# Kernel tuning notes

Hardware: AMD Instinct MI355X
Metric: run time of the kernel (lower is better)

The kernel has to match this reference:

```python
import jax, jax.numpy as jnp
import numpy as np

B, W, H, C = 8, 32, 32, 64   # batch, width, height, hidden_size
NH = 8                        # num_attention_heads
M = 32                        # max_position_embeddings
P = C // 2                    # position_embedding_size (query_positional_score=True)


def setup_inputs() -> dict:
    key = jax.random.key(0)
    ks = jax.random.split(key, 7)
    s = 0.02
    return {
        "hidden_states": jax.random.normal(ks[0], (B, W, H, C), dtype=jnp.float32),
        "row_emb": jax.random.normal(ks[1], (2 * M - 1, P), dtype=jnp.float32) * s,
        "col_emb": jax.random.normal(ks[2], (2 * M - 1, P), dtype=jnp.float32) * s,
        "Wq": jax.random.normal(ks[3], (NH * C, C), dtype=jnp.float32) * s,
        "bq": jnp.zeros((NH * C,), dtype=jnp.float32),
        "Wk": jax.random.normal(ks[4], (NH * C, C), dtype=jnp.float32) * s,
        "bk": jnp.zeros((NH * C,), dtype=jnp.float32),
        "Wv": jax.random.normal(ks[5], (C, NH * C), dtype=jnp.float32) * s,
        "bv": jnp.zeros((C,), dtype=jnp.float32),
    }


def reference(hidden_states, row_emb, col_emb, Wq, bq, Wk, bk, Wv, bv):
    b, w, h, c = hidden_states.shape
    nh = Wq.shape[0] // c
    half = c // 2
    center = row_emb.shape[0] // 2  # = max_position_embeddings - 1

    # projections: all_head_size = nh * c (per source: hidden_size * num_heads)
    q = (hidden_states @ Wq.T + bq).reshape(b, w, h, nh, c)
    k = (hidden_states @ Wk.T + bk).reshape(b, w, h, nh, c)

    # relative index tables: rel[i, j] = (j - i) + (M - 1)
    iw = jnp.arange(w)
    ih = jnp.arange(h)
    rel_w = iw[None, :] - iw[:, None] + center   # (w, w)
    rel_h = ih[None, :] - ih[:, None] + center   # (h, h)
    r_emb = row_emb[rel_w]  # (w, w, P)
    c_emb = col_emb[rel_h]  # (h, h, P)

    # positional scores: q split into row/col halves
    q_row = q[..., :half]
    q_col = q[..., half:]
    row_scores = jnp.einsum('bijhd,ikd->bijhk', q_row, r_emb)  # (b,w,h,nh,w)
    col_scores = jnp.einsum('bijhd,jld->bijhl', q_col, c_emb)  # (b,w,h,nh,h)
    scale = jnp.sqrt(jnp.asarray(c, dtype=hidden_states.dtype))
    scores = (row_scores[..., :, None] + col_scores[..., None, :]) / scale  # (b,w,h,nh,w,h)

    # content scores q^T k
    scores = scores + jnp.einsum('bijhd,bklhd->bijhkl', q, k) / scale

    # softmax over merged spatial key dims (k,l)
    probs = jax.nn.softmax(scores.reshape(b, w, h, nh, w * h), axis=-1).reshape(scores.shape)

    # value mixing directly with hidden_states, then output projection
    mixed = jnp.einsum('bijhkl,bkld->bijhd', probs, hidden_states).reshape(b, w, h, nh * c)
    return mixed @ Wv.T + bv
```

## Files before the change

### kernel.cpp

```cpp
#include <hip/hip_runtime.h>
#include <math.h>

typedef __bf16 bf16;
typedef bf16 bf16x2 __attribute__((ext_vector_type(2)));
typedef bf16 bf16x4 __attribute__((ext_vector_type(4)));
typedef bf16 bf16x8 __attribute__((ext_vector_type(8)));
typedef float f32x4 __attribute__((ext_vector_type(4)));

constexpr int CENTER = 31;

static __device__ __forceinline__ unsigned short f2bf_bits(float f) {
    bf16 b = (bf16)f;
    return __builtin_bit_cast(unsigned short, b);
}

__global__ __launch_bounds__(256)
void prep_kernel(const float* __restrict__ hid,
                 const float* __restrict__ Wq, const float* __restrict__ Wk,
                 const float* __restrict__ Wv,
                 bf16* __restrict__ hb, bf16* __restrict__ htb,
                 bf16* __restrict__ Wqb, bf16* __restrict__ Wkb,
                 bf16* __restrict__ Wvb)
{
    __shared__ __attribute__((aligned(16))) bf16 hs[64][72];

    const int t   = threadIdx.x;
    const int blk = blockIdx.x;
    const int b   = blk >> 4, kc = blk & 15;

    {
        int row = t >> 2, c4 = (t & 3) * 16;
        const float4* src = (const float4*)(hid + ((size_t)b * 1024 + kc * 64 + row) * 64 + c4);
        bf16 tmp[16];
        #pragma unroll
        for (int u = 0; u < 4; ++u) {
            float4 v = src[u];
            tmp[4*u+0] = (bf16)v.x; tmp[4*u+1] = (bf16)v.y;
            tmp[4*u+2] = (bf16)v.z; tmp[4*u+3] = (bf16)v.w;
        }
        *(int4*)&hs[row][c4]     = ((int4*)tmp)[0];
        *(int4*)&hs[row][c4 + 8] = ((int4*)tmp)[1];
        bf16* hdst = hb + ((size_t)b * 1024 + kc * 64 + row) * 64 + c4;
        *(int4*)hdst       = ((int4*)tmp)[0];
        *(int4*)(hdst + 8) = ((int4*)tmp)[1];
    }

    {
        int idx = blk * 256 + t;
        if (idx < 8192) {
            float4 vq = ((const float4*)Wq)[idx];
            float4 vk = ((const float4*)Wk)[idx];
            float4 vv = ((const float4*)Wv)[idx];
            ushort4 pq, pk2, pv;
            pq.x = f2bf_bits(vq.x); pq.y = f2bf_bits(vq.y); pq.z = f2bf_bits(vq.z); pq.w = f2bf_bits(vq.w);
            pk2.x = f2bf_bits(vk.x); pk2.y = f2bf_bits(vk.y); pk2.z = f2bf_bits(vk.z); pk2.w = f2bf_bits(vk.w);
            pv.x = f2bf_bits(vv.x); pv.y = f2bf_bits(vv.y); pv.z = f2bf_bits(vv.z); pv.w = f2bf_bits(vv.w);
            ((ushort4*)Wqb)[idx] = pq;
            ((ushort4*)Wkb)[idx] = pk2;
            ((ushort4*)Wvb)[idx] = pv;
        }
    }
    __syncthreads();

    {
        int d = t >> 2, p0 = (t & 3) * 16;
        ushort tmp[16];
        #pragma unroll
        for (int i = 0; i < 16; ++i)
            tmp[i] = __builtin_bit_cast(unsigned short, hs[p0 + i][d]);
        bf16* dst = htb + ((size_t)b * 64 + d) * 1024 + kc * 64 + p0;
        *(int4*)dst       = ((int4*)tmp)[0];
        *(int4*)(dst + 8) = ((int4*)tmp)[1];
    }
}

__global__ __launch_bounds__(256)
void qkproj_kernel(const bf16* __restrict__ hb,
                   const bf16* __restrict__ Wqb, const float* __restrict__ bq,
                   const bf16* __restrict__ Wkb, const float* __restrict__ bk,
                   bf16* __restrict__ qb, bf16* __restrict__ kb)
{
    __shared__ __attribute__((aligned(16))) bf16 As[128][72];
    __shared__ __attribute__((aligned(16))) bf16 Bqs[128][72];
    __shared__ __attribute__((aligned(16))) bf16 Bks[128][72];

    const int t  = threadIdx.x;
    const int pt = blockIdx.x;
    const int ot = blockIdx.y;
    const int p0 = pt * 128;
    const int b  = p0 >> 10;

    {
        int row = t >> 1, ch = (t & 1) * 32;
        const int4* asrc = (const int4*)(hb + (size_t)(p0 + row) * 64 + ch);
        const int4* qsrc = (const int4*)(Wqb + (size_t)(ot * 128 + row) * 64 + ch);
        const int4* ksrc = (const int4*)(Wkb + (size_t)(ot * 128 + row) * 64 + ch);
        #pragma unroll
        for (int u = 0; u < 4; ++u) {
            *(int4*)&As[row][ch + u * 8]  = asrc[u];
            *(int4*)&Bqs[row][ch + u * 8] = qsrc[u];
            *(int4*)&Bks[row][ch + u * 8] = ksrc[u];
        }
    }
    __syncthreads();

    const int w = t >> 6, ln = t & 63, l15 = ln & 15, quad = ln >> 4;

    bf16x8 a[2][2];
    #pragma unroll
    for (int mt = 0; mt < 2; ++mt) {
        a[mt][0] = *(const bf16x8*)&As[w * 32 + mt * 16 + l15][quad * 8];
        a[mt][1] = *(const bf16x8*)&As[w * 32 + mt * 16 + l15][32 + quad * 8];
    }

    const f32x4 z4 = {0.f, 0.f, 0.f, 0.f};

    for (int z = 0; z < 2; ++z) {
        const bf16 (* __restrict__ Bs)[72] = z ? Bks : Bqs;
        const float* bias = z ? bk : bq;
        bf16* outp        = z ? kb : qb;
        const float scale = z ? 1.0f : 0.125f;

        f32x4 acc[2][8];
        #pragma unroll
        for (int mt = 0; mt < 2; ++mt)
            #pragma unroll
            for (int nt = 0; nt < 8; ++nt) acc[mt][nt] = z4;

        #pragma unroll
        for (int nt = 0; nt < 8; ++nt) {
            bf16x8 b0 = *(const bf16x8*)&Bs[nt * 16 + l15][quad * 8];
            bf16x8 b1 = *(const bf16x8*)&Bs[nt * 16 + l15][32 + quad * 8];
            #pragma unroll
            for (int mt = 0; mt < 2; ++mt) {
                acc[mt][nt] = __builtin_amdgcn_mfma_f32_16x16x32_bf16(a[mt][0], b0, acc[mt][nt], 0, 0, 0);
                acc[mt][nt] = __builtin_amdgcn_mfma_f32_16x16x32_bf16(a[mt][1], b1, acc[mt][nt], 0, 0, 0);
            }
        }

        #pragma unroll
        for (int nt = 0; nt < 8; ++nt) {
            int o = ot * 128 + nt * 16 + l15;
            float bv = bias[o];
            int hh = o >> 6, d = o & 63;
            #pragma unroll
            for (int mt = 0; mt < 2; ++mt)
                #pragma unroll
                for (int r = 0; r < 4; ++r) {
                    int pos = (p0 & 1023) + w * 32 + mt * 16 + quad * 4 + r;
                    float val = (acc[mt][nt][r] + bv) * scale;
                    outp[(((size_t)b * 8 + hh) * 1024 + pos) * 64 + d] = (bf16)val;
                }
        }
    }
}

__global__ __launch_bounds__(256)
void bias_kernel(const bf16* __restrict__ qb,
                 const float* __restrict__ row_emb, const float* __restrict__ col_emb,
                 bf16* __restrict__ rowbias, bf16* __restrict__ colbias)
{
    __shared__ __attribute__((aligned(16))) bf16 embRs[63][40];
    __shared__ __attribute__((aligned(16))) bf16 embCs[63][40];

    const int t  = threadIdx.x;
    const int bh = blockIdx.x;
    const int sg = blockIdx.y;

    for (int i = t; i < 2016; i += 256) embRs[i >> 5][i & 31] = (bf16)row_emb[i];
    for (int i = t; i < 2016; i += 256) embCs[i >> 5][i & 31] = (bf16)col_emb[i];
    __syncthreads();

    const int w = t >> 6, ln = t & 63, l15 = ln & 15, quad = ln >> 4;

    #pragma unroll
    for (int u = 0; u < 4; ++u) {
        int s = sg * 16 + u * 4 + w;
        bool cm = s >= 32;
        int ij = cm ? s - 32 : s;

        bf16x8 a[2];
        #pragma unroll
        for (int mt = 0; mt < 2; ++mt) {
            const bf16* ap = cm
                ? qb + ((size_t)bh * 1024 + (mt * 16 + l15) * 32 + ij) * 64 + 32 + quad * 8
                : qb + ((size_t)bh * 1024 + ij * 32 + mt * 16 + l15) * 64 + quad * 8;
            a[mt] = *(const bf16x8*)ap;
        }
        bf16* ob = cm ? colbias : rowbias;

        #pragma unroll
        for (int nt = 0; nt < 2; ++nt) {
            int erow = nt * 16 + l15 + CENTER - ij;
            bf16x8 bfrag = cm ? *(const bf16x8*)&embCs[erow][quad * 8]
                              : *(const bf16x8*)&embRs[erow][quad * 8];
            #pragma unroll
            for (int mt = 0; mt < 2; ++mt) {
                f32x4 c = {0.f, 0.f, 0.f, 0.f};
                c = __builtin_amdgcn_mfma_f32_16x16x32_bf16(a[mt], bfrag, c, 0, 0, 0);
                #pragma unroll
                for (int r = 0; r < 4; ++r) {
                    int ql = mt * 16 + quad * 4 + r;
                    int qrow = cm ? ql * 32 + ij : ij * 32 + ql;
                    ob[((size_t)bh * 1024 + qrow) * 32 + nt * 16 + l15] = (bf16)c[r];
                }
            }
        }
    }
}

__global__ __launch_bounds__(256, 2)
void attn_kernel(const bf16* __restrict__ qb, const bf16* __restrict__ kb,
                 const bf16* __restrict__ htb,
                 const bf16* __restrict__ rowbias, const bf16* __restrict__ colbias,
                 bf16* __restrict__ mixedb)
{
    __shared__ __attribute__((aligned(16))) bf16 Ks[64][72];
    __shared__ __attribute__((aligned(16))) bf16 Hts[64][72];
    __shared__ __attribute__((aligned(16))) bf16 Pp[4][32][72];

    const int t  = threadIdx.x;
    const int qt = blockIdx.x;
    const int bh = blockIdx.y;
    const int b  = bh >> 3, h = bh & 7;
    const int q0 = qt * 128;
    const int w = t >> 6, ln = t & 63, l15 = ln & 15, quad = ln >> 4;

    bf16x8 bq_[2][2];
    float  cbv[2][2][4];
    const bf16* rbp[2];
    #pragma unroll
    for (int mt = 0; mt < 2; ++mt) {
        int qrow = q0 + w * 32 + mt * 16 + l15;
        const bf16* qp = qb + ((size_t)bh * 1024 + qrow) * 64;
        bq_[mt][0] = *(const bf16x8*)(qp + quad * 8);
        bq_[mt][1] = *(const bf16x8*)(qp + 32 + quad * 8);
        #pragma unroll
        for (int par = 0; par < 2; ++par) {
            bf16x4 cv = *(const bf16x4*)(colbias + ((size_t)bh * 1024 + qrow) * 32 + par * 16 + quad * 4);
            #pragma unroll
            for (int r = 0; r < 4; ++r) cbv[mt][par][r] = (float)cv[r];
        }
        rbp[mt] = rowbias + ((size_t)bh * 1024 + qrow) * 32;
    }

    const f32x4 z4 = {0.f, 0.f, 0.f, 0.f};
    f32x4 oacc[2][4];
    float lsum[2] = {0.f, 0.f};
    #pragma unroll
    for (int mt = 0; mt < 2; ++mt)
        #pragma unroll
        for (int dt = 0; dt < 4; ++dt) oacc[mt][dt] = z4;

    bf16* Pw = &Pp[w][0][0];
    const bf16* kcbase = kb + (size_t)bh * 1024 * 64;
    const bf16* hcbase = htb + (size_t)b * 64 * 1024;

    for (int kc = 0; kc < 16; ++kc) {
        __syncthreads();
        {
            int row = t >> 2, c = (t & 3) << 4;
            const bf16* ksrc = kcbase + (size_t)(kc * 64 + row) * 64 + c;
            *(int4*)&Ks[row][c]     = *(const int4*)ksrc;
            *(int4*)&Ks[row][c + 8] = *(const int4*)(ksrc + 8);
            const bf16* hsrc = hcbase + (size_t)row * 1024 + kc * 64 + c;
            *(int4*)&Hts[row][c]     = *(const int4*)hsrc;
            *(int4*)&Hts[row][c + 8] = *(const int4*)(hsrc + 8);
        }
        float rb[2][2];
        #pragma unroll
        for (int mt = 0; mt < 2; ++mt) {
            bf16x2 rv = *(const bf16x2*)(rbp[mt] + kc * 2);
            rb[mt][0] = (float)rv[0]; rb[mt][1] = (float)rv[1];
        }
        __syncthreads();

        f32x4 sf[2][4];
        #pragma unroll
        for (int mt = 0; mt < 2; ++mt)
            #pragma unroll
            for (int kt = 0; kt < 4; ++kt) sf[mt][kt] = z4;
        #pragma unroll
        for (int kt = 0; kt < 4; ++kt) {
            bf16x8 aK0 = *(const bf16x8*)&Ks[kt * 16 + l15][quad * 8];
            bf16x8 aK1 = *(const bf16x8*)&Ks[kt * 16 + l15][32 + quad * 8];
            #pragma unroll
            for (int mt = 0; mt < 2; ++mt) {
                sf[mt][kt] = __builtin_amdgcn_mfma_f32_16x16x32_bf16(aK0, bq_[mt][0], sf[mt][kt], 0, 0, 0);
                sf[mt][kt] = __builtin_amdgcn_mfma_f32_16x16x32_bf16(aK1, bq_[mt][1], sf[mt][kt], 0, 0, 0);
            }
        }

        #pragma unroll
        for (int mt = 0; mt < 2; ++mt)
            #pragma unroll
            for (int kt = 0; kt < 4; ++kt) {
                float rbv = rb[mt][kt >> 1];
                ushort4 pk;
                float p0 = __expf(sf[mt][kt][0] + rbv + cbv[mt][kt & 1][0]);
                float p1 = __expf(sf[mt][kt][1] + rbv + cbv[mt][kt & 1][1]);
                float p2 = __expf(sf[mt][kt][2] + rbv + cbv[mt][kt & 1][2]);
                float p3 = __expf(sf[mt][kt][3] + rbv + cbv[mt][kt & 1][3]);
                lsum[mt] += (p0 + p1) + (p2 + p3);
                pk.x = f2bf_bits(p0); pk.y = f2bf_bits(p1);
                pk.z = f2bf_bits(p2); pk.w = f2bf_bits(p3);
                *(ushort4*)&Pw[(mt * 16 + l15) * 72 + kt * 16 + quad * 4] = pk;
            }

        bf16x8 bp[2][2];
        #pragma unroll
        for (int mt = 0; mt < 2; ++mt) {
            bp[mt][0] = *(const bf16x8*)&Pw[(mt * 16 + l15) * 72 + quad * 8];
            bp[mt][1] = *(const bf16x8*)&Pw[(mt * 16 + l15) * 72 + 32 + quad * 8];
        }
        #pragma unroll
        for (int dt = 0; dt < 4; ++dt) {
            bf16x8 aH0 = *(const bf16x8*)&Hts[dt * 16 + l15][quad * 8];
            bf16x8 aH1 = *(const bf16x8*)&Hts[dt * 16 + l15][32 + quad * 8];
            #pragma unroll
            for (int mt = 0; mt < 2; ++mt) {
                oacc[mt][dt] = __builtin_amdgcn_mfma_f32_16x16x32_bf16(aH0, bp[mt][0], oacc[mt][dt], 0, 0, 0);
                oacc[mt][dt] = __builtin_amdgcn_mfma_f32_16x16x32_bf16(aH1, bp[mt][1], oacc[mt][dt], 0, 0, 0);
            }
        }
    }

    float inv[2];
    #pragma unroll
    for (int mt = 0; mt < 2; ++mt) {
        float v = lsum[mt];
        v += __shfl_xor(v, 16);
        v += __shfl_xor(v, 32);
        inv[mt] = 1.0f / v;
    }
    #pragma unroll
    for (int mt = 0; mt < 2; ++mt) {
        int pos = q0 + w * 32 + mt * 16 + l15;
        bf16* mb = mixedb + ((size_t)b * 1024 + pos) * 512 + h * 64;
        #pragma unroll
        for (int dt = 0; dt < 4; ++dt) {
            ushort4 pk;
            pk.x = f2bf_bits(oacc[mt][dt][0] * inv[mt]);
            pk.y = f2bf_bits(oacc[mt][dt][1] * inv[mt]);
            pk.z = f2bf_bits(oacc[mt][dt][2] * inv[mt]);
            pk.w = f2bf_bits(oacc[mt][dt][3] * inv[mt]);
            *(ushort4*)(mb + dt * 16 + quad * 4) = pk;
        }
    }
}

__global__ __launch_bounds__(256)
void out_proj_kernel(const bf16* __restrict__ mixedb,
                     const bf16* __restrict__ Wvb, const float* __restrict__ bv,
                     float* __restrict__ out)
{
    __shared__ __attribute__((aligned(16))) bf16 Wvs[64][264];

    const int t  = threadIdx.x;
    const int p0 = blockIdx.x * 64;
    const int w = t >> 6, ln = t & 63, l15 = ln & 15, quad = ln >> 4;

    f32x4 acc[4];
    #pragma unroll
    for (int nt = 0; nt < 4; ++nt) {
        float bvv = bv[nt * 16 + l15];
        acc[nt] = (f32x4){bvv, bvv, bvv, bvv};
    }

    const bf16* arow = mixedb + (size_t)(p0 + w * 16 + l15) * 512;

    for (int half = 0; half < 2; ++half) {
        __syncthreads();
        {
            int c = t >> 2, seg = (t & 3) * 64;
            const int4* src = (const int4*)(Wvb + (size_t)c * 512 + half * 256 + seg);
            #pragma unroll
            for (int u = 0; u < 8; ++u)
                *(int4*)&Wvs[c][seg + u * 8] = src[u];
        }
        __syncthreads();

        #pragma unroll
        for (int kc = 0; kc < 8; ++kc) {
            bf16x8 a = *(const bf16x8*)(arow + half * 256 + kc * 32 + quad * 8);
            #pragma unroll
            for (int nt = 0; nt < 4; ++nt) {
                bf16x8 bfrag = *(const bf16x8*)&Wvs[nt * 16 + l15][kc * 32 + quad * 8];
                acc[nt] = __builtin_amdgcn_mfma_f32_16x16x32_bf16(a, bfrag, acc[nt], 0, 0, 0);
            }
        }
    }

    #pragma unroll
    for (int nt = 0; nt < 4; ++nt)
        #pragma unroll
        for (int r = 0; r < 4; ++r)
            out[(size_t)(p0 + w * 16 + quad * 4 + r) * 64 + nt * 16 + l15] = acc[nt][r];
}

extern "C" void kernel_launch(void* const* d_in, const int* in_sizes, int n_in,
                              void* d_out, int out_size, void* d_ws, size_t ws_size,
                              hipStream_t stream)
{
    const float* hid     = (const float*)d_in[0];
    const float* row_emb = (const float*)d_in[1];
    const float* col_emb = (const float*)d_in[2];
    const float* Wq      = (const float*)d_in[3];
    const float* bq      = (const float*)d_in[4];
    const float* Wk      = (const float*)d_in[5];
    const float* bk      = (const float*)d_in[6];
    const float* Wv      = (const float*)d_in[7];
    const float* bv      = (const float*)d_in[8];
    float* out = (float*)d_out;

    bf16* qb      = (bf16*)d_ws;
    bf16* kb      = qb + (size_t)64 * 1024 * 64;
    bf16* htb     = kb + (size_t)64 * 1024 * 64;
    bf16* rowbias = htb + (size_t)8 * 64 * 1024;
    bf16* colbias = rowbias + (size_t)64 * 1024 * 32;
    bf16* mixedb  = colbias + (size_t)64 * 1024 * 32;
    bf16* hb      = mixedb + (size_t)8 * 1024 * 512;
    bf16* Wqb     = hb + (size_t)8 * 1024 * 64;
    bf16* Wkb     = Wqb + (size_t)512 * 64;
    bf16* Wvb     = Wkb + (size_t)512 * 64;

    prep_kernel<<<128, 256, 0, stream>>>(hid, Wq, Wk, Wv, hb, htb, Wqb, Wkb, Wvb);
    qkproj_kernel<<<dim3(64, 4), 256, 0, stream>>>(hb, Wqb, bq, Wkb, bk, qb, kb);
    bias_kernel<<<dim3(64, 4), 256, 0, stream>>>(qb, row_emb, col_emb, rowbias, colbias);
    attn_kernel<<<dim3(8, 64), 256, 0, stream>>>(qb, kb, htb, rowbias, colbias, mixedb);
    out_proj_kernel<<<128, 256, 0, stream>>>(mixedb, Wvb, bv, out);
}
```

Measured before the change: 131.5 us.

## Pre-pack H and Wv into MFMA fragment layout, double-buffer K tiles in attention

The prep kernel now writes the transposed hidden states and Wv in a fragment-packed layout, so each lane can load its MFMA operands straight from global memory. The attention kernel drops the shared-memory staging of H, double-buffers the K tiles with a register prefetch, needs only one barrier per iteration, and preloads all row-bias values once. out_proj removes its shared-memory Wv staging and uses smaller tiles over twice as many blocks. In exchange, H fragments are read redundantly from global memory (or cache) by every wave, and register pressure rises.

```diff
diff --git a/kernel.cpp b/kernel.cpp
--- a/kernel.cpp
+++ b/kernel.cpp
@@ -18,9 +18,9 @@
 void prep_kernel(const float* __restrict__ hid,
                  const float* __restrict__ Wq, const float* __restrict__ Wk,
                  const float* __restrict__ Wv,
-                 bf16* __restrict__ hb, bf16* __restrict__ htb,
+                 bf16* __restrict__ hb, bf16* __restrict__ htp,
                  bf16* __restrict__ Wqb, bf16* __restrict__ Wkb,
-                 bf16* __restrict__ Wvb)
+                 bf16* __restrict__ Wvp)
 {
     __shared__ __attribute__((aligned(16))) bf16 hs[64][72];
 
@@ -57,18 +57,22 @@
             pv.x = f2bf_bits(vv.x); pv.y = f2bf_bits(vv.y); pv.z = f2bf_bits(vv.z); pv.w = f2bf_bits(vv.w);
             ((ushort4*)Wqb)[idx] = pq;
             ((ushort4*)Wkb)[idx] = pk2;
-            ((ushort4*)Wvb)[idx] = pv;
+            int c = idx >> 7, o4 = (idx & 127) * 4;
+            size_t dst = (size_t)((c >> 4) * 16 + (o4 >> 5)) * 512 + (c & 15) * 32 + (o4 & 31);
+            *(ushort4*)(Wvp + dst) = pv;
         }
     }
     __syncthreads();
 
     {
-        int d = t >> 2, p0 = (t & 3) * 16;
+        int d = t >> 2, seg = (t & 3) * 16;
+        int dt = d >> 4, l15 = d & 15, half = seg >> 5;
         ushort tmp[16];
         #pragma unroll
         for (int i = 0; i < 16; ++i)
-            tmp[i] = __builtin_bit_cast(unsigned short, hs[p0 + i][d]);
-        bf16* dst = htb + ((size_t)b * 64 + d) * 1024 + kc * 64 + p0;
+            tmp[i] = __builtin_bit_cast(unsigned short, hs[seg + i][d]);
+        bf16* dst = htp + (size_t)b * 65536 + kc * 4096 + dt * 1024
+                        + half * 512 + l15 * 32 + (seg & 31);
         *(int4*)dst       = ((int4*)tmp)[0];
         *(int4*)(dst + 8) = ((int4*)tmp)[1];
     }
@@ -211,12 +215,11 @@
 
 __global__ __launch_bounds__(256, 2)
 void attn_kernel(const bf16* __restrict__ qb, const bf16* __restrict__ kb,
-                 const bf16* __restrict__ htb,
+                 const bf16* __restrict__ htp,
                  const bf16* __restrict__ rowbias, const bf16* __restrict__ colbias,
                  bf16* __restrict__ mixedb)
 {
-    __shared__ __attribute__((aligned(16))) bf16 Ks[64][72];
-    __shared__ __attribute__((aligned(16))) bf16 Hts[64][72];
+    __shared__ __attribute__((aligned(16))) bf16 Ks[2][64][72];
     __shared__ __attribute__((aligned(16))) bf16 Pp[4][32][72];
 
     const int t  = threadIdx.x;
@@ -228,7 +231,7 @@
 
     bf16x8 bq_[2][2];
     float  cbv[2][2][4];
-    const bf16* rbp[2];
+    bf16x8 rb8[2][4];
     #pragma unroll
     for (int mt = 0; mt < 2; ++mt) {
         int qrow = q0 + w * 32 + mt * 16 + l15;
@@ -241,7 +244,9 @@
             #pragma unroll
             for (int r = 0; r < 4; ++r) cbv[mt][par][r] = (float)cv[r];
         }
-        rbp[mt] = rowbias + ((size_t)bh * 1024 + qrow) * 32;
+        const bf16* rp = rowbias + ((size_t)bh * 1024 + qrow) * 32;
+        #pragma unroll
+        for (int u = 0; u < 4; ++u) rb8[mt][u] = *(const bf16x8*)(rp + u * 8);
     }
 
     const f32x4 z4 = {0.f, 0.f, 0.f, 0.f};
@@ -253,27 +258,36 @@
         for (int dt = 0; dt < 4; ++dt) oacc[mt][dt] = z4;
 
     bf16* Pw = &Pp[w][0][0];
-    const bf16* kcbase = kb + (size_t)bh * 1024 * 64;
-    const bf16* hcbase = htb + (size_t)b * 64 * 1024;
-
+    const bf16* kcbase = kb + (size_t)bh * 65536;
+    const bf16* hfrag  = htp + (size_t)b * 65536 + l15 * 32 + quad * 8;
+
+    const int srow = t >> 2, sc = (t & 3) << 4;
+    {
+        const bf16* ks0 = kcbase + (size_t)srow * 64 + sc;
+        *(int4*)&Ks[0][srow][sc]     = *(const int4*)ks0;
+        *(int4*)&Ks[0][srow][sc + 8] = *(const int4*)(ks0 + 8);
+    }
+    __syncthreads();
+
+    #pragma unroll 2
     for (int kc = 0; kc < 16; ++kc) {
-        __syncthreads();
+        const int cur = kc & 1, nxt = cur ^ 1;
+
+        int4 kpa, kpb;
+        if (kc < 15) {
+            const bf16* kpre = kcbase + (size_t)((kc + 1) * 64 + srow) * 64 + sc;
+            kpa = *(const int4*)kpre;
+            kpb = *(const int4*)(kpre + 8);
+        }
+        bf16x8 hA[4][2];
         {
-            int row = t >> 2, c = (t & 3) << 4;
-            const bf16* ksrc = kcbase + (size_t)(kc * 64 + row) * 64 + c;
-            *(int4*)&Ks[row][c]     = *(const int4*)ksrc;
-            *(int4*)&Ks[row][c + 8] = *(const int4*)(ksrc + 8);
-            const bf16* hsrc = hcbase + (size_t)row * 1024 + kc * 64 + c;
-            *(int4*)&Hts[row][c]     = *(const int4*)hsrc;
-            *(int4*)&Hts[row][c + 8] = *(const int4*)(hsrc + 8);
-        }
-        float rb[2][2];
-        #pragma unroll
-        for (int mt = 0; mt < 2; ++mt) {
-            bf16x2 rv = *(const bf16x2*)(rbp[mt] + kc * 2);
-            rb[mt][0] = (float)rv[0]; rb[mt][1] = (float)rv[1];
-        }
-        __syncthreads();
+            const bf16* hp = hfrag + kc * 4096;
+            #pragma unroll
+            for (int dt = 0; dt < 4; ++dt) {
+                hA[dt][0] = *(const bf16x8*)(hp + dt * 1024);
+                hA[dt][1] = *(const bf16x8*)(hp + dt * 1024 + 512);
+            }
+        }
 
         f32x4 sf[2][4];
         #pragma unroll
@@ -282,8 +296,8 @@
             for (int kt = 0; kt < 4; ++kt) sf[mt][kt] = z4;
         #pragma unroll
         for (int kt = 0; kt < 4; ++kt) {
-            bf16x8 aK0 = *(const bf16x8*)&Ks[kt * 16 + l15][quad * 8];
-            bf16x8 aK1 = *(const bf16x8*)&Ks[kt * 16 + l15][32 + quad * 8];
+            bf16x8 aK0 = *(const bf16x8*)&Ks[cur][kt * 16 + l15][quad * 8];
+            bf16x8 aK1 = *(const bf16x8*)&Ks[cur][kt * 16 + l15][32 + quad * 8];
             #pragma unroll
             for (int mt = 0; mt < 2; ++mt) {
                 sf[mt][kt] = __builtin_amdgcn_mfma_f32_16x16x32_bf16(aK0, bq_[mt][0], sf[mt][kt], 0, 0, 0);
@@ -292,10 +306,12 @@
         }
 
         #pragma unroll
-        for (int mt = 0; mt < 2; ++mt)
+        for (int mt = 0; mt < 2; ++mt) {
+            float rb0 = (float)rb8[mt][kc >> 2][(kc & 3) * 2];
+            float rb1 = (float)rb8[mt][kc >> 2][(kc & 3) * 2 + 1];
             #pragma unroll
             for (int kt = 0; kt < 4; ++kt) {
-                float rbv = rb[mt][kt >> 1];
+                float rbv = (kt & 2) ? rb1 : rb0;
                 ushort4 pk;
                 float p0 = __expf(sf[mt][kt][0] + rbv + cbv[mt][kt & 1][0]);
                 float p1 = __expf(sf[mt][kt][1] + rbv + cbv[mt][kt & 1][1]);
@@ -306,6 +322,7 @@
                 pk.z = f2bf_bits(p2); pk.w = f2bf_bits(p3);
                 *(ushort4*)&Pw[(mt * 16 + l15) * 72 + kt * 16 + quad * 4] = pk;
             }
+        }
 
         bf16x8 bp[2][2];
         #pragma unroll
@@ -315,14 +332,18 @@
         }
         #pragma unroll
         for (int dt = 0; dt < 4; ++dt) {
-            bf16x8 aH0 = *(const bf16x8*)&Hts[dt * 16 + l15][quad * 8];
-            bf16x8 aH1 = *(const bf16x8*)&Hts[dt * 16 + l15][32 + quad * 8];
             #pragma unroll
             for (int mt = 0; mt < 2; ++mt) {
-                oacc[mt][dt] = __builtin_amdgcn_mfma_f32_16x16x32_bf16(aH0, bp[mt][0], oacc[mt][dt], 0, 0, 0);
-                oacc[mt][dt] = __builtin_amdgcn_mfma_f32_16x16x32_bf16(aH1, bp[mt][1], oacc[mt][dt], 0, 0, 0);
-            }
-        }
+                oacc[mt][dt] = __builtin_amdgcn_mfma_f32_16x16x32_bf16(hA[dt][0], bp[mt][0], oacc[mt][dt], 0, 0, 0);
+                oacc[mt][dt] = __builtin_amdgcn_mfma_f32_16x16x32_bf16(hA[dt][1], bp[mt][1], oacc[mt][dt], 0, 0, 0);
+            }
+        }
+
+        if (kc < 15) {
+            *(int4*)&Ks[nxt][srow][sc]     = kpa;
+            *(int4*)&Ks[nxt][srow][sc + 8] = kpb;
+        }
+        __syncthreads();
     }
 
     float inv[2];
@@ -351,51 +372,34 @@
 
 __global__ __launch_bounds__(256)
 void out_proj_kernel(const bf16* __restrict__ mixedb,
-                     const bf16* __restrict__ Wvb, const float* __restrict__ bv,
+                     const bf16* __restrict__ Wvp, const float* __restrict__ bv,
                      float* __restrict__ out)
 {
-    __shared__ __attribute__((aligned(16))) bf16 Wvs[64][264];
-
     const int t  = threadIdx.x;
-    const int p0 = blockIdx.x * 64;
+    const int p0 = blockIdx.x * 32;
     const int w = t >> 6, ln = t & 63, l15 = ln & 15, quad = ln >> 4;
 
-    f32x4 acc[4];
-    #pragma unroll
-    for (int nt = 0; nt < 4; ++nt) {
-        float bvv = bv[nt * 16 + l15];
-        acc[nt] = (f32x4){bvv, bvv, bvv, bvv};
-    }
-
-    const bf16* arow = mixedb + (size_t)(p0 + w * 16 + l15) * 512;
-
-    for (int half = 0; half < 2; ++half) {
-        __syncthreads();
-        {
-            int c = t >> 2, seg = (t & 3) * 64;
-            const int4* src = (const int4*)(Wvb + (size_t)c * 512 + half * 256 + seg);
-            #pragma unroll
-            for (int u = 0; u < 8; ++u)
-                *(int4*)&Wvs[c][seg + u * 8] = src[u];
-        }
-        __syncthreads();
-
-        #pragma unroll
-        for (int kc = 0; kc < 8; ++kc) {
-            bf16x8 a = *(const bf16x8*)(arow + half * 256 + kc * 32 + quad * 8);
-            #pragma unroll
-            for (int nt = 0; nt < 4; ++nt) {
-                bf16x8 bfrag = *(const bf16x8*)&Wvs[nt * 16 + l15][kc * 32 + quad * 8];
-                acc[nt] = __builtin_amdgcn_mfma_f32_16x16x32_bf16(a, bfrag, acc[nt], 0, 0, 0);
-            }
-        }
-    }
-
-    #pragma unroll
-    for (int nt = 0; nt < 4; ++nt)
+    float bvv = bv[w * 16 + l15];
+    f32x4 acc[2] = {(f32x4){bvv, bvv, bvv, bvv}, (f32x4){bvv, bvv, bvv, bvv}};
+
+    const bf16* arow0 = mixedb + (size_t)(p0 + l15) * 512 + quad * 8;
+    const bf16* arow1 = mixedb + (size_t)(p0 + 16 + l15) * 512 + quad * 8;
+    const bf16* bbase = Wvp + (size_t)w * 16 * 512 + l15 * 32 + quad * 8;
+
+    #pragma unroll
+    for (int kc = 0; kc < 16; ++kc) {
+        bf16x8 a0 = *(const bf16x8*)(arow0 + kc * 32);
+        bf16x8 a1 = *(const bf16x8*)(arow1 + kc * 32);
+        bf16x8 bfrag = *(const bf16x8*)(bbase + kc * 512);
+        acc[0] = __builtin_amdgcn_mfma_f32_16x16x32_bf16(a0, bfrag, acc[0], 0, 0, 0);
+        acc[1] = __builtin_amdgcn_mfma_f32_16x16x32_bf16(a1, bfrag, acc[1], 0, 0, 0);
+    }
+
+    #pragma unroll
+    for (int mt = 0; mt < 2; ++mt)
         #pragma unroll
         for (int r = 0; r < 4; ++r)
-            out[(size_t)(p0 + w * 16 + quad * 4 + r) * 64 + nt * 16 + l15] = acc[nt][r];
+            out[(size_t)(p0 + mt * 16 + quad * 4 + r) * 64 + w * 16 + l15] = acc[mt][r];
 }
 
 extern "C" void kernel_launch(void* const* d_in, const int* in_sizes, int n_in,
@@ -415,18 +419,18 @@
 
     bf16* qb      = (bf16*)d_ws;
     bf16* kb      = qb + (size_t)64 * 1024 * 64;
-    bf16* htb     = kb + (size_t)64 * 1024 * 64;
-    bf16* rowbias = htb + (size_t)8 * 64 * 1024;
+    bf16* htp     = kb + (size_t)64 * 1024 * 64;
+    bf16* rowbias = htp + (size_t)8 * 64 * 1024;
     bf16* colbias = rowbias + (size_t)64 * 1024 * 32;
     bf16* mixedb  = colbias + (size_t)64 * 1024 * 32;
     bf16* hb      = mixedb + (size_t)8 * 1024 * 512;
     bf16* Wqb     = hb + (size_t)8 * 1024 * 64;
     bf16* Wkb     = Wqb + (size_t)512 * 64;
-    bf16* Wvb     = Wkb + (size_t)512 * 64;
-
-    prep_kernel<<<128, 256, 0, stream>>>(hid, Wq, Wk, Wv, hb, htb, Wqb, Wkb, Wvb);
+    bf16* Wvp     = Wkb + (size_t)512 * 64;
+
+    prep_kernel<<<128, 256, 0, stream>>>(hid, Wq, Wk, Wv, hb, htp, Wqb, Wkb, Wvp);
     qkproj_kernel<<<dim3(64, 4), 256, 0, stream>>>(hb, Wqb, bq, Wkb, bk, qb, kb);
     bias_kernel<<<dim3(64, 4), 256, 0, stream>>>(qb, row_emb, col_emb, rowbias, colbias);
-    attn_kernel<<<dim3(8, 64), 256, 0, stream>>>(qb, kb, htb, rowbias, colbias, mixedb);
-    out_proj_kernel<<<128, 256, 0, stream>>>(mixedb, Wvb, bv, out);
-}
+    attn_kernel<<<dim3(8, 64), 256, 0, stream>>>(qb, kb, htp, rowbias, colbias, mixedb);
+    out_proj_kernel<<<256, 256, 0, stream>>>(mixedb, Wvp, bv, out);
+}
```

After: 203.4 us. +54.7%, slower.

## Pre-pack Wv into MFMA fragment layout and drop LDS staging in output projection

Applied to the files above, without the earlier changes.

The prep kernel now writes bf16 Wv in a packed layout of 16-row by 32-column tiles, so each MFMA B fragment becomes one contiguous 16-byte global load. The output projection kernel drops the shared-memory staging of Wv and its barriers, reads fragments directly from global memory and L2, and gives each wave a 16-column output slice over 32 rows. The grid doubles to 256 blocks of 32 rows each to raise parallelism. In exchange, each mixedb row is now read by all four waves rather than once.

```diff
diff --git a/kernel.cpp b/kernel.cpp
--- a/kernel.cpp
+++ b/kernel.cpp
@@ -20,7 +20,7 @@
                  const float* __restrict__ Wv,
                  bf16* __restrict__ hb, bf16* __restrict__ htb,
                  bf16* __restrict__ Wqb, bf16* __restrict__ Wkb,
-                 bf16* __restrict__ Wvb)
+                 bf16* __restrict__ Wvp)
 {
     __shared__ __attribute__((aligned(16))) bf16 hs[64][72];
 
@@ -57,7 +57,9 @@
             pv.x = f2bf_bits(vv.x); pv.y = f2bf_bits(vv.y); pv.z = f2bf_bits(vv.z); pv.w = f2bf_bits(vv.w);
             ((ushort4*)Wqb)[idx] = pq;
             ((ushort4*)Wkb)[idx] = pk2;
-            ((ushort4*)Wvb)[idx] = pv;
+            int c = idx >> 7, o4 = (idx & 127) * 4;
+            size_t dst = (size_t)((c >> 4) * 16 + (o4 >> 5)) * 512 + (c & 15) * 32 + (o4 & 31);
+            *(ushort4*)(Wvp + dst) = pv;
         }
     }
     __syncthreads();
@@ -351,51 +353,34 @@
 
 __global__ __launch_bounds__(256)
 void out_proj_kernel(const bf16* __restrict__ mixedb,
-                     const bf16* __restrict__ Wvb, const float* __restrict__ bv,
+                     const bf16* __restrict__ Wvp, const float* __restrict__ bv,
                      float* __restrict__ out)
 {
-    __shared__ __attribute__((aligned(16))) bf16 Wvs[64][264];
-
     const int t  = threadIdx.x;
-    const int p0 = blockIdx.x * 64;
+    const int p0 = blockIdx.x * 32;
     const int w = t >> 6, ln = t & 63, l15 = ln & 15, quad = ln >> 4;
 
-    f32x4 acc[4];
-    #pragma unroll
-    for (int nt = 0; nt < 4; ++nt) {
-        float bvv = bv[nt * 16 + l15];
-        acc[nt] = (f32x4){bvv, bvv, bvv, bvv};
-    }
-
-    const bf16* arow = mixedb + (size_t)(p0 + w * 16 + l15) * 512;
-
-    for (int half = 0; half < 2; ++half) {
-        __syncthreads();
-        {
-            int c = t >> 2, seg = (t & 3) * 64;
-            const int4* src = (const int4*)(Wvb + (size_t)c * 512 + half * 256 + seg);
-            #pragma unroll
-            for (int u = 0; u < 8; ++u)
-                *(int4*)&Wvs[c][seg + u * 8] = src[u];
-        }
-        __syncthreads();
-
-        #pragma unroll
-        for (int kc = 0; kc < 8; ++kc) {
-            bf16x8 a = *(const bf16x8*)(arow + half * 256 + kc * 32 + quad * 8);
-            #pragma unroll
-            for (int nt = 0; nt < 4; ++nt) {
-                bf16x8 bfrag = *(const bf16x8*)&Wvs[nt * 16 + l15][kc * 32 + quad * 8];
-                acc[nt] = __builtin_amdgcn_mfma_f32_16x16x32_bf16(a, bfrag, acc[nt], 0, 0, 0);
-            }
-        }
-    }
-
-    #pragma unroll
-    for (int nt = 0; nt < 4; ++nt)
+    float bvv = bv[w * 16 + l15];
+    f32x4 acc[2] = {(f32x4){bvv, bvv, bvv, bvv}, (f32x4){bvv, bvv, bvv, bvv}};
+
+    const bf16* arow0 = mixedb + (size_t)(p0 + l15) * 512 + quad * 8;
+    const bf16* arow1 = mixedb + (size_t)(p0 + 16 + l15) * 512 + quad * 8;
+    const bf16* bbase = Wvp + (size_t)w * 16 * 512 + l15 * 32 + quad * 8;
+
+    #pragma unroll
+    for (int kc = 0; kc < 16; ++kc) {
+        bf16x8 a0 = *(const bf16x8*)(arow0 + kc * 32);
+        bf16x8 a1 = *(const bf16x8*)(arow1 + kc * 32);
+        bf16x8 bfrag = *(const bf16x8*)(bbase + kc * 512);
+        acc[0] = __builtin_amdgcn_mfma_f32_16x16x32_bf16(a0, bfrag, acc[0], 0, 0, 0);
+        acc[1] = __builtin_amdgcn_mfma_f32_16x16x32_bf16(a1, bfrag, acc[1], 0, 0, 0);
+    }
+
+    #pragma unroll
+    for (int mt = 0; mt < 2; ++mt)
         #pragma unroll
         for (int r = 0; r < 4; ++r)
-            out[(size_t)(p0 + w * 16 + quad * 4 + r) * 64 + nt * 16 + l15] = acc[nt][r];
+            out[(size_t)(p0 + mt * 16 + quad * 4 + r) * 64 + w * 16 + l15] = acc[mt][r];
 }
 
 extern "C" void kernel_launch(void* const* d_in, const int* in_sizes, int n_in,
@@ -422,11 +407,11 @@
     bf16* hb      = mixedb + (size_t)8 * 1024 * 512;
     bf16* Wqb     = hb + (size_t)8 * 1024 * 64;
     bf16* Wkb     = Wqb + (size_t)512 * 64;
-    bf16* Wvb     = Wkb + (size_t)512 * 64;
-
-    prep_kernel<<<128, 256, 0, stream>>>(hid, Wq, Wk, Wv, hb, htb, Wqb, Wkb, Wvb);
+    bf16* Wvp     = Wkb + (size_t)512 * 64;
+
+    prep_kernel<<<128, 256, 0, stream>>>(hid, Wq, Wk, Wv, hb, htb, Wqb, Wkb, Wvp);
     qkproj_kernel<<<dim3(64, 4), 256, 0, stream>>>(hb, Wqb, bq, Wkb, bk, qb, kb);
     bias_kernel<<<dim3(64, 4), 256, 0, stream>>>(qb, row_emb, col_emb, rowbias, colbias);
     attn_kernel<<<dim3(8, 64), 256, 0, stream>>>(qb, kb, htb, rowbias, colbias, mixedb);
-    out_proj_kernel<<<128, 256, 0, stream>>>(mixedb, Wvb, bv, out);
-}
+    out_proj_kernel<<<256, 256, 0, stream>>>(mixedb, Wvp, bv, out);
+}
```

After: 129.9 us, median of 2. About the same (-1.2%).
